# Kernel optimization log

Measured on AMD Instinct MI355X. Metric: run time of the kernel, lower is better.

Reference implementation:

```python
import jax, jax.numpy as jnp
import numpy as np

D_MODEL, D_K, D_V, BLOCK = 1024, 128, 128, 2048
B, T = 8, 2048

def setup_inputs() -> dict:
    key = jax.random.key(0)
    kx, kq, kk, kv = jax.random.split(key, 4)
    # nn.Linear weights are [out_features, in_features]
    s = 1.0 / np.sqrt(D_MODEL)
    return {
        "x": jax.random.normal(kx, (B, T, D_MODEL), dtype=jnp.float32),
        "W_q": jax.random.uniform(kq, (D_K, D_MODEL), jnp.float32, -s, s),
        "W_k": jax.random.uniform(kk, (D_K, D_MODEL), jnp.float32, -s, s),
        "W_v": jax.random.uniform(kv, (D_V, D_MODEL), jnp.float32, -s, s),
    }

def reference(x, W_q, W_k, W_v) -> jnp.ndarray:
    Tlen = x.shape[1]
    Q = jnp.einsum('btc,kc->btk', x, W_q)   # [B,T,d_k]
    K = jnp.einsum('btc,kc->btk', x, W_k)   # [B,T,d_k]
    V = jnp.einsum('btc,vc->btv', x, W_v)   # [B,T,d_v]
    scores = jnp.einsum('bqk,bsk->bqs', Q, K) / jnp.sqrt(jnp.float32(D_K))
    causal = jnp.tril(jnp.ones((Tlen, Tlen), dtype=bool))[None, :, :]
    scores = jnp.where(causal, scores, jnp.finfo(scores.dtype).min)
    attn = jax.nn.softmax(scores, axis=-1)
    return jnp.einsum('bqs,bsv->bqv', attn, V)  # [B,T,d_v]
```

## Files before the change

### kernel.cpp

```cpp
#include <hip/hip_runtime.h>
#include <hip/hip_fp16.h>

typedef _Float16 half8  __attribute__((ext_vector_type(8)));
typedef _Float16 half4v __attribute__((ext_vector_type(4)));
typedef float    f32x4  __attribute__((ext_vector_type(4)));

#define MFMA_F16 __builtin_amdgcn_mfma_f32_16x16x32_f16

#define BAR_LDS() asm volatile("s_waitcnt lgkmcnt(0)\n\ts_barrier" ::: "memory")
#define BAR_VM()  asm volatile("s_waitcnt vmcnt(0)\n\ts_barrier" ::: "memory")

__device__ __forceinline__ unsigned pack_f16(float a, float b) {
    union { __fp16 h __attribute__((ext_vector_type(2))); unsigned u; } cv;
    cv.h = __builtin_amdgcn_cvt_pkrtz(a, b);
    return cv.u;
}

__device__ __forceinline__ void gload16(const _Float16* g, _Float16* l) {
    __builtin_amdgcn_global_load_lds((const __attribute__((address_space(1))) void*)g,
                                     (__attribute__((address_space(3))) void*)l, 16, 0, 0);
}

__global__ __launch_bounds__(256) void cvt_k(const float* __restrict__ x,
                                             const float* __restrict__ wq,
                                             const float* __restrict__ wk,
                                             const float* __restrict__ wv,
                                             _Float16* __restrict__ xh,
                                             _Float16* __restrict__ wh) {
    int i = (blockIdx.x * 256 + threadIdx.x) * 8;
    const float* src;
    _Float16* dst;
    int off;
    if (i < 16777216) { src = x; dst = xh; off = i; }
    else {
        int j = i - 16777216;
        dst = wh; off = j;
        if (j < 131072)      { src = wq; }
        else if (j < 262144) { src = wk; off = j; }
        else                 { src = wv; off = j; }
        if (j < 131072)      { src = wq; }
        else if (j < 262144) { src = wk; j -= 131072; }
        else                 { src = wv; j -= 262144; }
        float4 a = *(const float4*)(src + j);
        float4 b = *(const float4*)(src + j + 4);
        half8 h;
        h[0]=(_Float16)a.x; h[1]=(_Float16)a.y; h[2]=(_Float16)a.z; h[3]=(_Float16)a.w;
        h[4]=(_Float16)b.x; h[5]=(_Float16)b.y; h[6]=(_Float16)b.z; h[7]=(_Float16)b.w;
        *(half8*)(dst + off) = h;
        return;
    }
    float4 a = *(const float4*)(src + off);
    float4 b = *(const float4*)(src + off + 4);
    half8 h;
    h[0]=(_Float16)a.x; h[1]=(_Float16)a.y; h[2]=(_Float16)a.z; h[3]=(_Float16)a.w;
    h[4]=(_Float16)b.x; h[5]=(_Float16)b.y; h[6]=(_Float16)b.z; h[7]=(_Float16)b.w;
    *(half8*)(dst + off) = h;
}

__global__ __launch_bounds__(256, 4) void qkv_k(const _Float16* __restrict__ xh,
                                                const _Float16* __restrict__ wh,
                                                _Float16* __restrict__ qh,
                                                _Float16* __restrict__ kh,
                                                _Float16* __restrict__ vth) {
    __shared__ _Float16 xs[2][64 * 128];
    const int tid = threadIdx.x;
    const int w = tid >> 6, l = tid & 63;
    const int fr = l & 15, fq = l >> 4;
    const int bid = blockIdx.x;
    const int xcd = bid & 7;
    const int slot = bid >> 3;
    const int rb = (slot / 3) * 8 + xcd;
    const int cb = slot % 3;
    const int row0 = rb * 64;
    const int c0 = cb * 128 + w * 32;
    const int xwk = (fr & 7) << 4;

    int srow[4], scol[4];
#pragma unroll
    for (int i = 0; i < 4; ++i) {
        int ob = w * 4096 + i * 1024 + l * 16;
        srow[i] = ob >> 8;
        scol[i] = ((ob & 255) ^ ((srow[i] & 7) << 4)) >> 1;
    }
    const _Float16* wgb = wh + (c0 + fr) * 1024 + fq * 8;

    f32x4 acc[4][2] = {};
    half8 wf[4][2];

#define GLX(kt, bb) do {                                                                  \
    _Pragma("unroll")                                                                     \
    for (int i = 0; i < 4; ++i)                                                           \
        gload16(xh + (row0 + srow[i]) * 1024 + (kt) * 128 + scol[i],                      \
                &xs[bb][0] + w * 2048 + i * 512);                                         \
    } while (0)

#pragma unroll
    for (int ss = 0; ss < 3; ++ss)
#pragma unroll
        for (int nf = 0; nf < 2; ++nf)
            wf[ss][nf] = *(const half8*)(wgb + nf * 16384 + ss * 32);
    GLX(0, 0);
    BAR_VM();
    GLX(1, 1);

    int cur = 0;
    for (int kt = 0; kt < 8; ++kt) {
#pragma unroll
        for (int s = 0; s < 4; ++s) {
            const int ss = kt * 4 + s;
            if (ss + 3 < 32) {
#pragma unroll
                for (int nf = 0; nf < 2; ++nf)
                    wf[(ss + 3) & 3][nf] = *(const half8*)(wgb + nf * 16384 + (ss + 3) * 32);
            }
            half8 af[4];
#pragma unroll
            for (int mf = 0; mf < 4; ++mf) {
                const char* rp = (const char*)(&xs[cur][0]) + (mf * 16 + fr) * 256;
                af[mf] = *(const half8*)(rp + ((s * 64 + fq * 16) ^ xwk));
            }
#pragma unroll
            for (int mf = 0; mf < 4; ++mf)
#pragma unroll
                for (int nf = 0; nf < 2; ++nf)
                    acc[mf][nf] = MFMA_F16(af[mf], wf[ss & 3][nf], acc[mf][nf], 0, 0, 0);
        }
        BAR_VM();
        if (kt + 2 < 8) GLX(kt + 2, cur);
        cur ^= 1;
    }
#undef GLX

#pragma unroll
    for (int nf = 0; nf < 2; ++nf) {
        int n0 = c0 + nf * 16 + fr;
#pragma unroll
        for (int mf = 0; mf < 4; ++mf) {
            int mb = row0 + mf * 16 + fq * 4;
            if (cb == 0) {
#pragma unroll
                for (int r = 0; r < 4; ++r) qh[(mb + r) * 128 + n0] = (_Float16)acc[mf][nf][r];
            } else if (cb == 1) {
#pragma unroll
                for (int r = 0; r < 4; ++r) kh[(mb + r) * 128 + (n0 - 128)] = (_Float16)acc[mf][nf][r];
            } else {
                half4v pv;
#pragma unroll
                for (int r = 0; r < 4; ++r) pv[r] = (_Float16)acc[mf][nf][r];
                int t = mb & 2047;
                int tl = t & 63;
                int tp = (t & ~63) | (tl & 35) | ((tl & 12) << 1) | ((tl & 16) >> 2);
                *(half4v*)(&vth[((mb >> 11) * 128 + (n0 - 256)) * 2048 + tp]) = pv;
            }
        }
    }
}

__global__ __launch_bounds__(512, 4) void attn_k(const _Float16* __restrict__ qh,
                                                 const _Float16* __restrict__ kh,
                                                 const _Float16* __restrict__ vth,
                                                 _Float16* __restrict__ part,
                                                 float* __restrict__ stats,
                                                 float* __restrict__ out) {
    __shared__ _Float16 ks[2][32 * 128];
    __shared__ _Float16 vs[2][128 * 32];

    int bid = blockIdx.x;
    int b = bid & 7;
    int u = bid >> 3;
    int qt, c;
    {
        int idx = u;
        qt = 0;
        for (;;) { int nc = (qt >> 1) + 1; if (idx < nc) break; idx -= nc; ++qt; }
        c = idx;
    }
    int j0 = c * 8;
    int jmax = 4 * qt + 4;
    int j1 = j0 + 8 < jmax ? j0 + 8 : jmax;

    int tid = threadIdx.x, w = tid >> 6, l = tid & 63;
    int fr = l & 15, fq = l >> 4;
    int xw = (fr & 7) << 4;
    int xv = (fr & 3) << 4;

    const int kr  = tid >> 4;
    const int kc  = (tid & 15) ^ (kr & 7);
    const int vdd = tid >> 2;
    const int vc  = (tid & 3) ^ (vdd & 3);

    half8 qf[4];
    const _Float16* qp = qh + ((b * 2048 + qt * 128 + w * 16 + fr) << 7);
#pragma unroll
    for (int cc = 0; cc < 4; ++cc) qf[cc] = *(const half8*)(qp + cc * 32 + fq * 8);

#define GLOAD_TILE(j, bb) do {                                                            \
    gload16(kh + (((b << 11) + ((j) << 5) + kr) << 7) + kc * 8, &ks[bb][0] + w * 512);    \
    gload16(vth + (((b << 7) + vdd) << 11) + ((j) << 5) + vc * 8, &vs[bb][0] + w * 512);  \
    } while (0)

    f32x4 acc[8] = {};
    float mrow = -1e30f, lrow = 0.0f;

    GLOAD_TILE(j0, 0);
    BAR_VM();
    if (j0 + 1 < j1) GLOAD_TILE(j0 + 1, 1);

    int cur = 0;
    for (int j = j0; j < j1; ++j) {
        const char* ksb = (const char*)(ks[cur]);
        const char* vsb = (const char*)(vs[cur]);

        f32x4 s[2] = {};
        __builtin_amdgcn_s_setprio(1);
#pragma unroll
        for (int n = 0; n < 2; ++n) {
            const char* krow = ksb + (n * 16 + fr) * 256;
#pragma unroll
            for (int cc = 0; cc < 4; ++cc) {
                half8 kf = *(const half8*)(krow + ((cc * 64 + fq * 16) ^ xw));
                s[n] = MFMA_F16(kf, qf[cc], s[n], 0, 0, 0);
            }
        }
        __builtin_amdgcn_s_setprio(0);
        const float sc = 0.088388347648318447f;
        if (j >= 4 * qt) {
            int koff = (j - 4 * qt) << 5;
            int qrow = w * 16 + fr;
#pragma unroll
            for (int n = 0; n < 2; ++n)
#pragma unroll
                for (int r = 0; r < 4; ++r) {
                    int kcol = koff + n * 16 + fq * 4 + r;
                    float v = s[n][r] * sc;
                    s[n][r] = (kcol > qrow) ? -1e30f : v;
                }
        } else {
#pragma unroll
            for (int n = 0; n < 2; ++n)
#pragma unroll
                for (int r = 0; r < 4; ++r) s[n][r] *= sc;
        }

        float pmax = s[0][0];
#pragma unroll
        for (int n = 0; n < 2; ++n)
#pragma unroll
            for (int r = 0; r < 4; ++r) pmax = fmaxf(pmax, s[n][r]);
        float al = 1.0f;
        if (!__all(pmax - mrow <= 8.0f)) {
            float mx = pmax;
            mx = fmaxf(mx, __shfl_xor(mx, 16));
            mx = fmaxf(mx, __shfl_xor(mx, 32));
            float nm = fmaxf(mrow, mx);
            al = __expf(mrow - nm);
            mrow = nm;
#pragma unroll
            for (int dt = 0; dt < 8; ++dt)
#pragma unroll
                for (int r = 0; r < 4; ++r) acc[dt][r] *= al;
        }
        float rs = 0.f;
#pragma unroll
        for (int n = 0; n < 2; ++n)
#pragma unroll
            for (int r = 0; r < 4; ++r) {
                float p = __expf(s[n][r] - mrow);
                s[n][r] = p;
                rs += p;
            }
        rs += __shfl_xor(rs, 16);
        rs += __shfl_xor(rs, 32);
        lrow = lrow * al + rs;

        union { unsigned u[4]; half8 h; } pb;
        pb.u[0] = pack_f16(s[0][0], s[0][1]);
        pb.u[1] = pack_f16(s[0][2], s[0][3]);
        pb.u[2] = pack_f16(s[1][0], s[1][1]);
        pb.u[3] = pack_f16(s[1][2], s[1][3]);

        __builtin_amdgcn_s_setprio(1);
#pragma unroll
        for (int dt = 0; dt < 8; ++dt) {
            const char* vrow = vsb + (dt * 16 + fr) * 64;
            half8 vf = *(const half8*)(vrow + ((fq * 16) ^ xv));
            acc[dt] = MFMA_F16(vf, pb.h, acc[dt], 0, 0, 0);
        }
        __builtin_amdgcn_s_setprio(0);

        BAR_VM();
        if (j + 2 < j1) GLOAD_TILE(j + 2, cur);
        cur ^= 1;
    }

    float inv = 1.0f / lrow;

    if (qt < 2) {
        float* op = out + ((b * 2048 + qt * 128 + w * 16 + fr) << 7) + fq * 4;
#pragma unroll
        for (int dt = 0; dt < 8; ++dt) {
            float4 o;
            o.x = acc[dt][0] * inv; o.y = acc[dt][1] * inv;
            o.z = acc[dt][2] * inv; o.w = acc[dt][3] * inv;
            *(float4*)(op + dt * 16) = o;
        }
    } else {
        _Float16* op = part + bid * 16384 + w * 2048 + l * 4;
#pragma unroll
        for (int dt = 0; dt < 8; ++dt) {
            half4v h;
#pragma unroll
            for (int r = 0; r < 4; ++r) h[r] = (_Float16)(acc[dt][r] * inv);
            *(half4v*)(op + dt * 256) = h;
        }
        if (l < 16) {
            int ridx = bid * 128 + w * 16 + l;
            float2 st; st.x = mrow; st.y = lrow;
            *(float2*)(&stats[ridx * 2]) = st;
        }
    }
#undef GLOAD_TILE
}

__global__ __launch_bounds__(256) void comb_k(const _Float16* __restrict__ part,
                                              const float* __restrict__ stats,
                                              float* __restrict__ out) {
    int bid = blockIdx.x;
    int b = bid & 7;
    int rest = bid >> 3;
    int qt = 2 + (rest >> 2);
    int rh = rest & 3;
    int h = qt >> 1;
    int nc = h + 1;
    int u0 = qt + h * (h - 1) + (qt & 1) * h;
    int t = threadIdx.x;
    int row = rh * 32 + (t >> 3), g = t & 7;
    int w = row >> 4, q16 = row & 15;

    float mstar = -1e30f, mv[8], lv[8];
#pragma unroll
    for (int cc = 0; cc < 8; ++cc) {
        if (cc < nc) {
            int sidx = (((u0 + cc) << 3) + b) * 128 + row;
            mv[cc] = stats[sidx * 2];
            lv[cc] = stats[sidx * 2 + 1];
            mstar = fmaxf(mstar, mv[cc]);
        }
    }
    float den = 0.f, wc[8];
#pragma unroll
    for (int cc = 0; cc < 8; ++cc) {
        if (cc < nc) { wc[cc] = __expf(mv[cc] - mstar) * lv[cc]; den += wc[cc]; }
        else wc[cc] = 0.f;
    }
    float a[16] = {};
#pragma unroll
    for (int cc = 0; cc < 8; ++cc) {
        if (cc < nc) {
            const _Float16* pp = part + ((((u0 + cc) << 3) + b) * 16384) + w * 2048 + g * 256;
            float wcc = wc[cc];
#pragma unroll
            for (int fq = 0; fq < 4; ++fq) {
                half4v hh = *(const half4v*)(pp + (fq * 16 + q16) * 4);
#pragma unroll
                for (int r = 0; r < 4; ++r)
                    a[fq * 4 + r] += wcc * (float)hh[r];
            }
        }
    }
    float id = 1.0f / den;
    float* op = out + (b * 2048 + qt * 128 + row) * 128 + g * 16;
#pragma unroll
    for (int uu = 0; uu < 4; ++uu) {
        float4 o;
        o.x = a[uu * 4]     * id;
        o.y = a[uu * 4 + 1] * id;
        o.z = a[uu * 4 + 2] * id;
        o.w = a[uu * 4 + 3] * id;
        *(float4*)(op + uu * 4) = o;
    }
}

extern "C" void kernel_launch(void* const* d_in, const int* in_sizes, int n_in,
                              void* d_out, int out_size, void* d_ws, size_t ws_size,
                              hipStream_t stream) {
    const float* x  = (const float*)d_in[0];
    const float* wq = (const float*)d_in[1];
    const float* wk = (const float*)d_in[2];
    const float* wv = (const float*)d_in[3];

    char* ws = (char*)d_ws;
    _Float16* wh   = (_Float16*)(ws);
    _Float16* qhp  = (_Float16*)(ws + (1u  << 20));
    _Float16* khp  = (_Float16*)(ws + (5u  << 20));
    _Float16* vtp  = (_Float16*)(ws + (9u  << 20));
    _Float16* part = (_Float16*)(ws + (13u << 20));
    float*    stat = (float*)   (ws + (32u << 20));
    _Float16* xhp  = (_Float16*)(ws + (34u << 20));

    cvt_k<<<8384, 256, 0, stream>>>(x, wq, wk, wv, xhp, wh);
    qkv_k<<<768, 256, 0, stream>>>(xhp, wh, qhp, khp, vtp);
    attn_k<<<576, 512, 0, stream>>>(qhp, khp, vtp, part, stat, (float*)d_out);
    comb_k<<<448, 256, 0, stream>>>(part, stat, (float*)d_out);
}
```

Measured before the change: 84.40 us.

## Fuse fp32-to-fp16 conversion of x into the QKV projection kernel

Drops the separate pass that converted all of x to fp16 and stored it in workspace. The QKV kernel now streams fp32 x tiles directly into LDS and packs them to fp16 on the fly before the MFMA. The conversion kernel shrinks to handle only the weights. This removes a full read and write of x (64MB fp32 in, 32MB fp16 out) plus the re-read of the fp16 copy. In exchange the projection kernel reads x as fp32, runs twice as many K-tile iterations, does more LDS traffic and cvt work, and keeps a shallower weight prefetch.

```diff
diff --git a/kernel.cpp b/kernel.cpp
--- a/kernel.cpp
+++ b/kernel.cpp
@@ -16,53 +16,34 @@
     return cv.u;
 }
 
-__device__ __forceinline__ void gload16(const _Float16* g, _Float16* l) {
+__device__ __forceinline__ void gload16(const void* g, void* l) {
     __builtin_amdgcn_global_load_lds((const __attribute__((address_space(1))) void*)g,
                                      (__attribute__((address_space(3))) void*)l, 16, 0, 0);
 }
 
-__global__ __launch_bounds__(256) void cvt_k(const float* __restrict__ x,
-                                             const float* __restrict__ wq,
-                                             const float* __restrict__ wk,
-                                             const float* __restrict__ wv,
-                                             _Float16* __restrict__ xh,
-                                             _Float16* __restrict__ wh) {
+__global__ __launch_bounds__(256) void wconv_k(const float* __restrict__ wq,
+                                               const float* __restrict__ wk,
+                                               const float* __restrict__ wv,
+                                               _Float16* __restrict__ wh) {
     int i = (blockIdx.x * 256 + threadIdx.x) * 8;
-    const float* src;
-    _Float16* dst;
-    int off;
-    if (i < 16777216) { src = x; dst = xh; off = i; }
-    else {
-        int j = i - 16777216;
-        dst = wh; off = j;
-        if (j < 131072)      { src = wq; }
-        else if (j < 262144) { src = wk; off = j; }
-        else                 { src = wv; off = j; }
-        if (j < 131072)      { src = wq; }
-        else if (j < 262144) { src = wk; j -= 131072; }
-        else                 { src = wv; j -= 262144; }
-        float4 a = *(const float4*)(src + j);
-        float4 b = *(const float4*)(src + j + 4);
-        half8 h;
-        h[0]=(_Float16)a.x; h[1]=(_Float16)a.y; h[2]=(_Float16)a.z; h[3]=(_Float16)a.w;
-        h[4]=(_Float16)b.x; h[5]=(_Float16)b.y; h[6]=(_Float16)b.z; h[7]=(_Float16)b.w;
-        *(half8*)(dst + off) = h;
-        return;
-    }
+    const float* src; int off;
+    if (i < 131072)      { src = wq; off = i; }
+    else if (i < 262144) { src = wk; off = i - 131072; }
+    else                 { src = wv; off = i - 262144; }
     float4 a = *(const float4*)(src + off);
     float4 b = *(const float4*)(src + off + 4);
     half8 h;
     h[0]=(_Float16)a.x; h[1]=(_Float16)a.y; h[2]=(_Float16)a.z; h[3]=(_Float16)a.w;
     h[4]=(_Float16)b.x; h[5]=(_Float16)b.y; h[6]=(_Float16)b.z; h[7]=(_Float16)b.w;
-    *(half8*)(dst + off) = h;
-}
-
-__global__ __launch_bounds__(256, 4) void qkv_k(const _Float16* __restrict__ xh,
+    *(half8*)(wh + i) = h;
+}
+
+__global__ __launch_bounds__(256, 4) void qkv_k(const float* __restrict__ x,
                                                 const _Float16* __restrict__ wh,
                                                 _Float16* __restrict__ qh,
                                                 _Float16* __restrict__ kh,
                                                 _Float16* __restrict__ vth) {
-    __shared__ _Float16 xs[2][64 * 128];
+    __shared__ float xs[2][64 * 64];
     const int tid = threadIdx.x;
     const int w = tid >> 6, l = tid & 63;
     const int fr = l & 15, fq = l >> 4;
@@ -75,58 +56,63 @@
     const int c0 = cb * 128 + w * 32;
     const int xwk = (fr & 7) << 4;
 
-    int srow[4], scol[4];
+    int srow[4], scolB[4];
 #pragma unroll
     for (int i = 0; i < 4; ++i) {
-        int ob = w * 4096 + i * 1024 + l * 16;
-        srow[i] = ob >> 8;
-        scol[i] = ((ob & 255) ^ ((srow[i] & 7) << 4)) >> 1;
+        int ob = i * 4096 + w * 1024 + l * 16;
+        srow[i]  = ob >> 8;
+        scolB[i] = (ob & 255) ^ ((srow[i] & 7) << 4);
     }
     const _Float16* wgb = wh + (c0 + fr) * 1024 + fq * 8;
 
     f32x4 acc[4][2] = {};
-    half8 wf[4][2];
+    half8 wf[2][2];
 
 #define GLX(kt, bb) do {                                                                  \
     _Pragma("unroll")                                                                     \
     for (int i = 0; i < 4; ++i)                                                           \
-        gload16(xh + (row0 + srow[i]) * 1024 + (kt) * 128 + scol[i],                      \
-                &xs[bb][0] + w * 2048 + i * 512);                                         \
+        gload16(x + (row0 + srow[i]) * 1024 + (kt) * 64 + (scolB[i] >> 2),                \
+                (char*)(&xs[bb][0]) + i * 4096 + w * 1024);                               \
     } while (0)
 
 #pragma unroll
-    for (int ss = 0; ss < 3; ++ss)
-#pragma unroll
-        for (int nf = 0; nf < 2; ++nf)
-            wf[ss][nf] = *(const half8*)(wgb + nf * 16384 + ss * 32);
+    for (int nf = 0; nf < 2; ++nf) wf[0][nf] = *(const half8*)(wgb + nf * 16384);
     GLX(0, 0);
     BAR_VM();
     GLX(1, 1);
 
     int cur = 0;
-    for (int kt = 0; kt < 8; ++kt) {
-#pragma unroll
-        for (int s = 0; s < 4; ++s) {
-            const int ss = kt * 4 + s;
-            if (ss + 3 < 32) {
+    for (int kt = 0; kt < 16; ++kt) {
+#pragma unroll
+        for (int s = 0; s < 2; ++s) {
+            const int ss = kt * 2 + s;
+            if (ss + 1 < 32) {
 #pragma unroll
                 for (int nf = 0; nf < 2; ++nf)
-                    wf[(ss + 3) & 3][nf] = *(const half8*)(wgb + nf * 16384 + (ss + 3) * 32);
+                    wf[(ss + 1) & 1][nf] = *(const half8*)(wgb + nf * 16384 + (ss + 1) * 32);
             }
             half8 af[4];
 #pragma unroll
             for (int mf = 0; mf < 4; ++mf) {
                 const char* rp = (const char*)(&xs[cur][0]) + (mf * 16 + fr) * 256;
-                af[mf] = *(const half8*)(rp + ((s * 64 + fq * 16) ^ xwk));
+                const int X = s * 128 + fq * 32;
+                float4 a0 = *(const float4*)(rp + (X ^ xwk));
+                float4 a1 = *(const float4*)(rp + ((X + 16) ^ xwk));
+                union { unsigned u[4]; half8 h; } cv;
+                cv.u[0] = pack_f16(a0.x, a0.y);
+                cv.u[1] = pack_f16(a0.z, a0.w);
+                cv.u[2] = pack_f16(a1.x, a1.y);
+                cv.u[3] = pack_f16(a1.z, a1.w);
+                af[mf] = cv.h;
             }
 #pragma unroll
             for (int mf = 0; mf < 4; ++mf)
 #pragma unroll
                 for (int nf = 0; nf < 2; ++nf)
-                    acc[mf][nf] = MFMA_F16(af[mf], wf[ss & 3][nf], acc[mf][nf], 0, 0, 0);
+                    acc[mf][nf] = MFMA_F16(af[mf], wf[ss & 1][nf], acc[mf][nf], 0, 0, 0);
         }
         BAR_VM();
-        if (kt + 2 < 8) GLX(kt + 2, cur);
+        if (kt + 2 < 16) GLX(kt + 2, cur);
         cur ^= 1;
     }
 #undef GLX
@@ -396,10 +382,9 @@
     _Float16* vtp  = (_Float16*)(ws + (9u  << 20));
     _Float16* part = (_Float16*)(ws + (13u << 20));
     float*    stat = (float*)   (ws + (32u << 20));
-    _Float16* xhp  = (_Float16*)(ws + (34u << 20));
-
-    cvt_k<<<8384, 256, 0, stream>>>(x, wq, wk, wv, xhp, wh);
-    qkv_k<<<768, 256, 0, stream>>>(xhp, wh, qhp, khp, vtp);
+
+    wconv_k<<<192, 256, 0, stream>>>(wq, wk, wv, wh);
+    qkv_k<<<768, 256, 0, stream>>>(x, wh, qhp, khp, vtp);
     attn_k<<<576, 512, 0, stream>>>(qhp, khp, vtp, part, stat, (float*)d_out);
     comb_k<<<448, 256, 0, stream>>>(part, stat, (float*)d_out);
 }
```

After: 78.94 us. 6.5% less time.
